# Optimization experiments

Measured on AMD Instinct MI355X. Metric: run time of the kernel, lower is better.

Reference implementation:

```python
import jax, jax.numpy as jnp
import numpy as np
from jax import lax

B, C, L, G = 2048, 9605, 20, 50
ALPHA, ALPHA1, ALPHA2, ALPHA3, ALPHA_OTHER = 0.5, 0.05, 2.0, 10.0, 0.5
NEG_INF = jnp.float32(-1e30)


def setup_inputs() -> dict:
    k0, k1, k2, k3 = jax.random.split(jax.random.key(0), 4)
    x = jax.random.normal(k0, (B, C), jnp.float32)
    # sparse multi-label targets (~10 positives/row) so at most ~1 whitelist group is active,
    # matching the original code's assert len(gt_whitelist_index) == 1
    y = (jax.random.uniform(k1, (B, C)) < 0.001).astype(jnp.int32)
    y_neg = (jax.random.uniform(k2, (B, C)) < 0.001).astype(jnp.int32)
    # L disjoint whitelist groups of G classes each (from mapping_dict in the original)
    idx = jax.random.permutation(k3, C)[: L * G].reshape(L, G)
    group_mask = jnp.zeros((L, C), bool).at[jnp.arange(L)[:, None], idx].set(True)
    return {"x": x, "y": y, "y_neg": y_neg, "group_mask": group_mask}


def _rank_loss(x1, x2, margin):
    # our_rank_loss: sigmoid(alpha3*(x2-x1+margin)), scaled by alpha2 when positive
    d = x2 - x1 + margin
    s = jax.nn.sigmoid(ALPHA3 * d)
    return jnp.where(d > 0, ALPHA2 * s, s)


def reference(x, y, y_neg, group_mask):
    xs = jax.nn.sigmoid(x)  # [B, C]
    gmf = group_mask.astype(jnp.float32)  # [L, C]

    # per-row max score inside each whitelist group -> [B, L]
    # lax.map over the L (=20) groups keeps peak memory at one [B, C] temp per step
    group_max = lax.map(
        lambda m: jnp.max(jnp.where(m, xs, NEG_INF), axis=-1), group_mask
    ).T  # [B, L]

    # find_gt_whitelist: group k active iff sum(y[group_k]) > 0
    active = jnp.einsum("bc,lc->bl", y.astype(jnp.float32), gmf) > 0
    active_neg = jnp.einsum("bc,lc->bl", y_neg.astype(jnp.float32), gmf) > 0
    has_gt = jnp.any(active, axis=-1)  # [B]
    g = jnp.argmax(active, axis=-1)  # first active group (original asserts exactly one)

    # top_k_thres = max(11th largest sigmoid score, alpha_other) in both branches
    thres = jnp.maximum(lax.top_k(xs, 11)[0][:, 10], ALPHA_OTHER)  # [B]

    # max over union of all whitelist classes (wl_indices)
    union_max = jnp.max(jnp.where(jnp.any(group_mask, 0)[None, :], xs, NEG_INF), -1)

    gt_max = jnp.take_along_axis(group_max, g[:, None], axis=1)[:, 0]  # [B]
    # incorrect_max: max(0, max over groups != g); incorrect_neg: max(0, max over neg-active groups)
    excl = jnp.where(jnp.arange(L)[None, :] == g[:, None], NEG_INF, group_max)
    incorrect_max = jnp.maximum(jnp.max(excl, -1), 0.0)
    incorrect_neg = jnp.maximum(jnp.max(jnp.where(active_neg, group_max, 0.0), -1), 0.0)

    # branch A: no gt whitelist group active
    case_a = (1 - ALPHA) * _rank_loss(thres, union_max, ALPHA1) + ALPHA * _rank_loss(
        thres, incorrect_neg, ALPHA1
    )
    # branch B: exactly one gt group g
    case_b = (
        _rank_loss(gt_max, thres, ALPHA1)
        + jnp.where(
            incorrect_max > 0, (1 - ALPHA) * _rank_loss(thres, incorrect_max, ALPHA1), 0.0
        )
        + jnp.where(
            incorrect_neg > 0,
            ALPHA * _rank_loss(thres, incorrect_neg, ALPHA1),
            ALPHA * _rank_loss(thres, incorrect_max, ALPHA1),
        )
    )
    return jnp.sum(jnp.where(has_gt, case_b, case_a))
```

## Files before the change

kernel.cpp:

```cpp
#include <hip/hip_runtime.h>
#include <stdint.h>

#define B_ROWS 2048
#define C_CLS  9605
#define L_GRP  20
#define GM_BYTES (L_GRP * C_CLS)
#define REPSTRIDE 9728
#define NEG_BIG -3.0e38f

__device__ __forceinline__ float sigmoidf(float v) {
  return 1.0f / (1.0f + __expf(-v));
}

__device__ __forceinline__ float rank_loss(float x1, float x2) {
  float d = x2 - x1 + 0.05f;
  float s = 1.0f / (1.0f + __expf(-10.0f * d));
  return d > 0.0f ? 2.0f * s : s;
}

__device__ __forceinline__ unsigned fmap(float f) {
  unsigned u = __float_as_uint(f);
  return (u & 0x80000000u) ? ~u : (u | 0x80000000u);
}
__device__ __forceinline__ float funmap(unsigned m) {
  unsigned u = (m & 0x80000000u) ? (m ^ 0x80000000u) : ~m;
  return __uint_as_float(u);
}

__global__ void probe_init_kernel(const uint4* __restrict__ gm,
                                  unsigned char* __restrict__ ws,
                                  float* __restrict__ out,
                                  int* __restrict__ flag) {
  __shared__ int s_part[16];
  const int tid = threadIdx.x;
  if (tid == 0) out[0] = 0.0f;
  const int initbytes = 3 * REPSTRIDE + C_CLS + 16;
  for (int i = tid; i < initbytes; i += 1024) ws[64 + i] = 0xFF;
  int local = 0;
  const int nvec = GM_BYTES / 16;
  for (int i = tid; i < nvec; i += 1024) {
    uint4 w = gm[i];
    unsigned a[4] = {w.x, w.y, w.z, w.w};
#pragma unroll
    for (int q = 0; q < 4; ++q) {
      local += ((a[q] & 0x000000FFu) != 0) + ((a[q] & 0x0000FF00u) != 0) +
               ((a[q] & 0x00FF0000u) != 0) + ((a[q] & 0xFF000000u) != 0);
    }
  }
  if (tid == 0) {
    const unsigned char* gb = (const unsigned char*)gm;
    for (int i = nvec * 16; i < GM_BYTES; ++i) local += (gb[i] != 0);
  }
#pragma unroll
  for (int off = 32; off; off >>= 1) local += __shfl_xor(local, off);
  if ((tid & 63) == 0) s_part[tid >> 6] = local;
  __syncthreads();
  if (tid == 0) {
    int tot = 0;
    for (int w = 0; w < 16; ++w) tot += s_part[w];
    *flag = tot;
  }
}

__global__ void build_gid_kernel(const void* gm, const int* __restrict__ flag,
                                 unsigned char* __restrict__ ws) {
  int i = blockIdx.x * blockDim.x + threadIdx.x;
  if (i >= GM_BYTES) return;
  const bool is_byte = (*flag > 600);
  bool m;
  if (is_byte) m = ((const unsigned char*)gm)[i] != 0;
  else         m = ((const unsigned int*)gm)[i] != 0u;
  if (m) {
    int l = i / C_CLS;
    int c = i - l * C_CLS;
    unsigned char* base = ws + 64;
#pragma unroll
    for (int r = 0; r < 4; ++r) base[r * REPSTRIDE + r + c] = (unsigned char)l;
  }
}

__global__ __launch_bounds__(256, 4) void loss_kernel(
    const float* __restrict__ x, const int* __restrict__ y,
    const int* __restrict__ yn, const unsigned char* __restrict__ ws64,
    float* __restrict__ out) {
  __shared__ unsigned s_gmax[L_GRP];
  __shared__ unsigned s_act, s_actn;
  __shared__ float s_wtop[4 * 11];
  const int tid = threadIdx.x;
  const int lane = tid & 63;
  const int wave = tid >> 6;
  const int row = blockIdx.x;

  const size_t base = (size_t)row * C_CLS;
  const int mis = (int)(base & 3);
  const int peel = (4 - mis) & 3;
  const float* xr = x + base;
  const int* yr = y + base;
  const int* nr = yn + base;
  const unsigned char* gidc = ws64 + mis * REPSTRIDE + mis;

  if (tid < L_GRP) s_gmax[tid] = 0u;
  if (tid == 0) { s_act = 0u; s_actn = 0u; }
  __syncthreads();

  float t[11];
#pragma unroll
  for (int i = 0; i < 11; ++i) t[i] = NEG_BIG;
  unsigned actL = 0u, actnL = 0u;

  auto process = [&](float v, unsigned gk, int yv, int nv) {
    if (v > t[10]) {
      float a = v;
#pragma unroll
      for (int i = 0; i < 11; ++i) {
        float hi = fmaxf(t[i], a); a = fminf(t[i], a); t[i] = hi;
      }
    }
    if (gk < L_GRP) {
      atomicMax(&s_gmax[gk], fmap(v));
      unsigned bit = 1u << gk;
      if (yv != 0) actL |= bit;
      if (nv != 0) actnL |= bit;
    }
  };

  if (tid < peel) process(xr[tid], gidc[tid], yr[tid], nr[tid]);

  const int nvec = (C_CLS - peel) >> 2;
  const float4* x4 = (const float4*)(xr + peel);
  const int4* y4 = (const int4*)(yr + peel);
  const int4* n4 = (const int4*)(nr + peel);
  const unsigned* g4 = (const unsigned*)(gidc + peel);
  for (int j = tid; j < nvec; j += 256) {
    float4 xv = x4[j];
    int4 yv = y4[j];
    int4 nv = n4[j];
    unsigned gw = g4[j];
    process(xv.x, gw & 0xFFu, yv.x, nv.x);
    process(xv.y, (gw >> 8) & 0xFFu, yv.y, nv.y);
    process(xv.z, (gw >> 16) & 0xFFu, yv.z, nv.z);
    process(xv.w, gw >> 24, yv.w, nv.w);
  }
  const int tail0 = peel + (nvec << 2);
  const int rem = C_CLS - tail0;
  if (tid < rem) {
    int c = tail0 + tid;
    process(xr[c], gidc[c], yr[c], nr[c]);
  }

  if (actL) atomicOr(&s_act, actL);
  if (actnL) atomicOr(&s_actn, actnL);

  float cur = t[0];
  float mr[11];
#pragma unroll
  for (int r = 0; r < 11; ++r) {
    float m = cur;
#pragma unroll
    for (int off = 32; off; off >>= 1) m = fmaxf(m, __shfl_xor(m, off));
    mr[r] = m;
    if (r < 10) {
      unsigned long long b = __ballot(cur == m);
      int leader = (int)(__ffsll(b) - 1);
      if (lane == leader) {
#pragma unroll
        for (int i = 0; i < 10; ++i) t[i] = t[i + 1];
        t[10] = NEG_BIG;
        cur = t[0];
      }
    }
  }
  if (lane == 0) {
#pragma unroll
    for (int r = 0; r < 11; ++r) s_wtop[wave * 11 + r] = mr[r];
  }
  __syncthreads();

  if (wave == 0) {
    float v = (lane < 44) ? s_wtop[lane] : NEG_BIG;
    float eleventh = NEG_BIG;
#pragma unroll
    for (int r = 0; r < 11; ++r) {
      float m = v;
#pragma unroll
      for (int off = 32; off; off >>= 1) m = fmaxf(m, __shfl_xor(m, off));
      eleventh = m;
      if (r < 10) {
        unsigned long long b = __ballot(v == m);
        int leader = (int)(__ffsll(b) - 1);
        if (lane == leader) v = NEG_BIG;
      }
    }

    const unsigned aL = s_act, anL = s_actn;
    const bool has_gt = (aL != 0u);
    const int g = has_gt ? (__ffs(aL) - 1) : 0;
    const float thres = fmaxf(sigmoidf(eleventh), 0.5f);

    float union_max = NEG_BIG, gt_sg = 0.0f, inc_max = NEG_BIG, inc_neg = 0.0f;
#pragma unroll
    for (int l = 0; l < L_GRP; ++l) {
      float sg = sigmoidf(funmap(s_gmax[l]));
      union_max = fmaxf(union_max, sg);
      if (l == g) gt_sg = sg; else inc_max = fmaxf(inc_max, sg);
      if ((anL >> l) & 1u) inc_neg = fmaxf(inc_neg, sg);
    }
    inc_max = fmaxf(inc_max, 0.0f);
    inc_neg = fmaxf(inc_neg, 0.0f);

    float loss;
    if (has_gt) {
      loss = rank_loss(gt_sg, thres);
      if (inc_max > 0.0f) loss += 0.5f * rank_loss(thres, inc_max);
      loss += 0.5f * rank_loss(thres, (inc_neg > 0.0f) ? inc_neg : inc_max);
    } else {
      loss = 0.5f * rank_loss(thres, union_max) + 0.5f * rank_loss(thres, inc_neg);
    }
    if (lane == 0) atomicAdd(out, loss);
  }
}

extern "C" void kernel_launch(void* const* d_in, const int* in_sizes, int n_in,
                              void* d_out, int out_size, void* d_ws, size_t ws_size,
                              hipStream_t stream) {
  (void)in_sizes; (void)n_in; (void)out_size; (void)ws_size;
  const float* x = (const float*)d_in[0];
  const int* y = (const int*)d_in[1];
  const int* yn = (const int*)d_in[2];
  const void* gm = d_in[3];

  int* flag = (int*)d_ws;
  unsigned char* ws = (unsigned char*)d_ws;
  unsigned char* ws64 = ws + 64;

  probe_init_kernel<<<1, 1024, 0, stream>>>((const uint4*)gm, ws,
                                            (float*)d_out, flag);
  build_gid_kernel<<<(GM_BYTES + 255) / 256, 256, 0, stream>>>(gm, flag, ws);
  loss_kernel<<<B_ROWS, 256, 0, stream>>>(x, y, yn, ws64, (float*)d_out);
}
```

Measured before the change: 253.3 us.

## Split loss pass into top-k, whitelist gather, and sparse label scan

The per-row kernel no longer handles group max, top-k and label bits together for every class. A compact list of (class, group) whitelist entries is built once. Each row then runs three passes: a top-k pass over x that rejects whole float4s below the current 11th value, an atomicMax gather over only the whitelist entries, and a y/y_neg scan that looks up the group id only when a label is nonzero. The top-k buffer now starts at 0 instead of -inf, which is safe because the threshold is clamped to sigmoid(0)=0.5. The aim is to cut per-element branching, byte loads and shared atomics. The cost is some re-reading of x through the gather and a global atomic counter in the build kernel.

New measurement: 282.9 us. 11.7% more time.

```diff
diff --git a/kernel.cpp b/kernel.cpp
--- a/kernel.cpp
+++ b/kernel.cpp
@@ -5,8 +5,10 @@
 #define C_CLS  9605
 #define L_GRP  20
 #define GM_BYTES (L_GRP * C_CLS)
-#define REPSTRIDE 9728
+#define GID_PAD 9728
+#define WL_CAP  7168
 #define NEG_BIG -3.0e38f
+
 
 __device__ __forceinline__ float sigmoidf(float v) {
   return 1.0f / (1.0f + __expf(-v));
@@ -33,9 +35,12 @@
                                   int* __restrict__ flag) {
   __shared__ int s_part[16];
   const int tid = threadIdx.x;
-  if (tid == 0) out[0] = 0.0f;
-  const int initbytes = 3 * REPSTRIDE + C_CLS + 16;
-  for (int i = tid; i < initbytes; i += 1024) ws[64 + i] = 0xFF;
+  if (tid == 0) {
+    out[0] = 0.0f;
+    *(int*)(ws + 8) = 0;
+  }
+  unsigned* gfill = (unsigned*)(ws + 64);
+  for (int i = tid; i < GID_PAD / 4; i += 1024) gfill[i] = 0xFFFFFFFFu;
   int local = 0;
   const int nvec = GM_BYTES / 16;
   for (int i = tid; i < nvec; i += 1024) {
@@ -73,15 +78,16 @@
   if (m) {
     int l = i / C_CLS;
     int c = i - l * C_CLS;
-    unsigned char* base = ws + 64;
-#pragma unroll
-    for (int r = 0; r < 4; ++r) base[r * REPSTRIDE + r + c] = (unsigned char)l;
+    ws[64 + c] = (unsigned char)l;
+    int p = atomicAdd((int*)(ws + 8), 1);
+    if (p < WL_CAP)
+      ((unsigned*)(ws + 64 + GID_PAD))[p] = (unsigned)c | ((unsigned)l << 16);
   }
 }
 
 __global__ __launch_bounds__(256, 4) void loss_kernel(
     const float* __restrict__ x, const int* __restrict__ y,
-    const int* __restrict__ yn, const unsigned char* __restrict__ ws64,
+    const int* __restrict__ yn, const unsigned char* __restrict__ ws,
     float* __restrict__ out) {
   __shared__ unsigned s_gmax[L_GRP];
   __shared__ unsigned s_act, s_actn;
@@ -97,7 +103,10 @@
   const float* xr = x + base;
   const int* yr = y + base;
   const int* nr = yn + base;
-  const unsigned char* gidc = ws64 + mis * REPSTRIDE + mis;
+  const unsigned char* gid = ws + 64;
+  const unsigned* wlist = (const unsigned*)(ws + 64 + GID_PAD);
+  int wl_n = *(const int*)(ws + 8);
+  if (wl_n > WL_CAP) wl_n = WL_CAP;
 
   if (tid < L_GRP) s_gmax[tid] = 0u;
   if (tid == 0) { s_act = 0u; s_actn = 0u; }
@@ -105,10 +114,10 @@
 
   float t[11];
 #pragma unroll
-  for (int i = 0; i < 11; ++i) t[i] = NEG_BIG;
+  for (int i = 0; i < 11; ++i) t[i] = 0.0f;
   unsigned actL = 0u, actnL = 0u;
 
-  auto process = [&](float v, unsigned gk, int yv, int nv) {
+  auto ins = [&](float v) {
     if (v > t[10]) {
       float a = v;
 #pragma unroll
@@ -116,36 +125,77 @@
         float hi = fmaxf(t[i], a); a = fminf(t[i], a); t[i] = hi;
       }
     }
-    if (gk < L_GRP) {
-      atomicMax(&s_gmax[gk], fmap(v));
-      unsigned bit = 1u << gk;
-      if (yv != 0) actL |= bit;
-      if (nv != 0) actnL |= bit;
-    }
   };
-
-  if (tid < peel) process(xr[tid], gidc[tid], yr[tid], nr[tid]);
-
+  auto edge = [&](int c) {
+    ins(xr[c]);
+    int yv = yr[c], nv = nr[c];
+    if (yv | nv) {
+      unsigned g = gid[c];
+      if (g < L_GRP) {
+        unsigned bit = 1u << g;
+        if (yv) actL |= bit;
+        if (nv) actnL |= bit;
+      }
+    }
+  };
+
+  if (tid < peel) edge(tid);
   const int nvec = (C_CLS - peel) >> 2;
+  const int tail0 = peel + (nvec << 2);
+  if (tid < C_CLS - tail0) edge(tail0 + tid);
+
   const float4* x4 = (const float4*)(xr + peel);
   const int4* y4 = (const int4*)(yr + peel);
   const int4* n4 = (const int4*)(nr + peel);
-  const unsigned* g4 = (const unsigned*)(gidc + peel);
-  for (int j = tid; j < nvec; j += 256) {
-    float4 xv = x4[j];
-    int4 yv = y4[j];
-    int4 nv = n4[j];
-    unsigned gw = g4[j];
-    process(xv.x, gw & 0xFFu, yv.x, nv.x);
-    process(xv.y, (gw >> 8) & 0xFFu, yv.y, nv.y);
-    process(xv.z, (gw >> 16) & 0xFFu, yv.z, nv.z);
-    process(xv.w, gw >> 24, yv.w, nv.w);
-  }
-  const int tail0 = peel + (nvec << 2);
-  const int rem = C_CLS - tail0;
-  if (tid < rem) {
-    int c = tail0 + tid;
-    process(xr[c], gidc[c], yr[c], nr[c]);
+
+  {
+    auto bodyA = [&](float4 a) {
+      float am = fmaxf(fmaxf(a.x, a.y), fmaxf(a.z, a.w));
+      if (am > t[10]) { ins(a.x); ins(a.y); ins(a.z); ins(a.w); }
+    };
+    int j = tid;
+    for (; j + 768 < nvec; j += 1024) {
+      float4 a = x4[j];
+      float4 b = x4[j + 256];
+      float4 c = x4[j + 512];
+      float4 d = x4[j + 768];
+      bodyA(a); bodyA(b); bodyA(c); bodyA(d);
+    }
+    for (; j < nvec; j += 256) bodyA(x4[j]);
+  }
+
+  for (int i = tid; i < wl_n; i += 256) {
+    unsigned e = wlist[i];
+    int c = (int)(e & 0xFFFFu);
+    unsigned g = e >> 16;
+    atomicMax(&s_gmax[g], fmap(xr[c]));
+  }
+
+  {
+    auto bodyB = [&](int j) {
+      int4 yv = y4[j];
+      int4 nv = n4[j];
+      int any = yv.x | yv.y | yv.z | yv.w | nv.x | nv.y | nv.z | nv.w;
+      if (any) {
+        int c0 = peel + (j << 2);
+        const int yq[4] = {yv.x, yv.y, yv.z, yv.w};
+        const int nq[4] = {nv.x, nv.y, nv.z, nv.w};
+#pragma unroll
+        for (int q = 0; q < 4; ++q) {
+          if (yq[q] | nq[q]) {
+            unsigned g = gid[c0 + q];
+            if (g < L_GRP) {
+              unsigned bit = 1u << g;
+              if (yq[q]) actL |= bit;
+              if (nq[q]) actnL |= bit;
+            }
+          }
+        }
+      }
+    };
+    int j = tid;
+    for (; j + 256 < nvec; j += 512) { bodyB(j); bodyB(j + 256); }
+    if (j < nvec) bodyB(j);
   }
 
   if (actL) atomicOr(&s_act, actL);
@@ -231,10 +281,9 @@
 
   int* flag = (int*)d_ws;
   unsigned char* ws = (unsigned char*)d_ws;
-  unsigned char* ws64 = ws + 64;
 
   probe_init_kernel<<<1, 1024, 0, stream>>>((const uint4*)gm, ws,
                                             (float*)d_out, flag);
   build_gid_kernel<<<(GM_BYTES + 255) / 256, 256, 0, stream>>>(gm, flag, ws);
-  loss_kernel<<<B_ROWS, 256, 0, stream>>>(x, y, yn, ws64, (float*)d_out);
-}
+  loss_kernel<<<B_ROWS, 256, 0, stream>>>(x, y, yn, ws, (float*)d_out);
+}
```

## Skip redundant top-k inserts and atomics, prefetch next row chunk in main loop

Applied to the files above, without the earlier changes.

Seeds the per-thread top-11 list at 0 instead of a huge negative value. Because the threshold is clamped to sigmoid(0)=0.5, any logit below zero can never matter, so far fewer insertions happen. A whole float4 quad is skipped when its max is under the current 11th value. Shared-memory atomicMax calls are skipped for quads with no whitelist class and for values that cannot raise the stored max. The y/y_neg active-group bookkeeping is skipped for all-zero quads, and the next iteration's loads are issued before the current quad is processed. The cost is more branching and extra live registers for the prefetched data, which could lower occupancy.

Measured after the change: 258.4 us. Within noise of the previous version (+2.0%).

```diff
diff --git a/kernel.cpp b/kernel.cpp
--- a/kernel.cpp
+++ b/kernel.cpp
@@ -105,10 +105,10 @@
 
   float t[11];
 #pragma unroll
-  for (int i = 0; i < 11; ++i) t[i] = NEG_BIG;
+  for (int i = 0; i < 11; ++i) t[i] = 0.0f;
   unsigned actL = 0u, actnL = 0u;
 
-  auto process = [&](float v, unsigned gk, int yv, int nv) {
+  auto ins = [&](float v) {
     if (v > t[10]) {
       float a = v;
 #pragma unroll
@@ -116,36 +116,76 @@
         float hi = fmaxf(t[i], a); a = fminf(t[i], a); t[i] = hi;
       }
     }
+  };
+  auto gmax_upd = [&](unsigned gk, float v) {
+    unsigned fm = fmap(v);
+    if (fm > s_gmax[gk]) atomicMax(&s_gmax[gk], fm);
+  };
+  auto edge = [&](int c) {
+    float v = xr[c];
+    ins(v);
+    unsigned gk = gidc[c];
     if (gk < L_GRP) {
-      atomicMax(&s_gmax[gk], fmap(v));
+      gmax_upd(gk, v);
       unsigned bit = 1u << gk;
-      if (yv != 0) actL |= bit;
-      if (nv != 0) actnL |= bit;
+      if (yr[c] != 0) actL |= bit;
+      if (nr[c] != 0) actnL |= bit;
     }
   };
 
-  if (tid < peel) process(xr[tid], gidc[tid], yr[tid], nr[tid]);
-
+  if (tid < peel) edge(tid);
   const int nvec = (C_CLS - peel) >> 2;
+  const int tail0 = peel + (nvec << 2);
+  if (tid < C_CLS - tail0) edge(tail0 + tid);
+
   const float4* x4 = (const float4*)(xr + peel);
   const int4* y4 = (const int4*)(yr + peel);
   const int4* n4 = (const int4*)(nr + peel);
   const unsigned* g4 = (const unsigned*)(gidc + peel);
-  for (int j = tid; j < nvec; j += 256) {
-    float4 xv = x4[j];
-    int4 yv = y4[j];
-    int4 nv = n4[j];
-    unsigned gw = g4[j];
-    process(xv.x, gw & 0xFFu, yv.x, nv.x);
-    process(xv.y, (gw >> 8) & 0xFFu, yv.y, nv.y);
-    process(xv.z, (gw >> 16) & 0xFFu, yv.z, nv.z);
-    process(xv.w, gw >> 24, yv.w, nv.w);
-  }
-  const int tail0 = peel + (nvec << 2);
-  const int rem = C_CLS - tail0;
-  if (tid < rem) {
-    int c = tail0 + tid;
-    process(xr[c], gidc[c], yr[c], nr[c]);
+
+  int j = tid;
+  if (j < nvec) {
+    float4 xa = x4[j];
+    int4 ya = y4[j];
+    int4 na = n4[j];
+    unsigned ga = g4[j];
+    for (;;) {
+      const int jn = j + 256;
+      const bool more = jn < nvec;
+      float4 xb; int4 yb, nb; unsigned gb;
+      if (more) {
+        xb = x4[jn]; yb = y4[jn]; nb = n4[jn]; gb = g4[jn];
+      }
+
+      if (ga != 0xFFFFFFFFu) {
+        unsigned g0 = ga & 0xFFu, g1 = (ga >> 8) & 0xFFu,
+                 g2 = (ga >> 16) & 0xFFu, g3 = ga >> 24;
+        if (g0 < L_GRP) gmax_upd(g0, xa.x);
+        if (g1 < L_GRP) gmax_upd(g1, xa.y);
+        if (g2 < L_GRP) gmax_upd(g2, xa.z);
+        if (g3 < L_GRP) gmax_upd(g3, xa.w);
+      }
+      if (ya.x | ya.y | ya.z | ya.w | na.x | na.y | na.z | na.w) {
+        const int yq[4] = {ya.x, ya.y, ya.z, ya.w};
+        const int nq[4] = {na.x, na.y, na.z, na.w};
+        const unsigned gq[4] = {ga & 0xFFu, (ga >> 8) & 0xFFu,
+                                (ga >> 16) & 0xFFu, ga >> 24};
+#pragma unroll
+        for (int q = 0; q < 4; ++q) {
+          if ((yq[q] | nq[q]) && gq[q] < L_GRP) {
+            unsigned bit = 1u << gq[q];
+            if (yq[q]) actL |= bit;
+            if (nq[q]) actnL |= bit;
+          }
+        }
+      }
+      float am = fmaxf(fmaxf(xa.x, xa.y), fmaxf(xa.z, xa.w));
+      if (am > t[10]) { ins(xa.x); ins(xa.y); ins(xa.z); ins(xa.w); }
+
+      if (!more) break;
+      j = jn;
+      xa = xb; ya = yb; na = nb; ga = gb;
+    }
   }
 
   if (actL) atomicOr(&s_act, actL);
```
